# Performance work log

Measured on AMD Instinct MI355X. Metric: run time of the kernel, lower is better.

## Reference

```python
import jax, jax.numpy as jnp
import numpy as np

N_SRC = 100_000
N_DST = 100_000
N_EDGES = 1_600_000
D_IN = 256
N_HEADS = 4
OUT_FEATS = 32
NEG_SLOPE = 0.2


def setup_inputs() -> dict:
    key = jax.random.key(0)
    k1, k2, k3, k4, k5, k6, k7 = jax.random.split(key, 7)
    return {
        "feat_src": jax.random.normal(k1, (N_SRC, D_IN), dtype=jnp.float32),
        "feat_dst": jax.random.normal(k2, (N_DST, D_IN), dtype=jnp.float32),
        "w_src": jax.random.normal(k3, (D_IN, N_HEADS * OUT_FEATS), dtype=jnp.float32) * 0.05,
        "w_dst": jax.random.normal(k4, (D_IN, N_HEADS * OUT_FEATS), dtype=jnp.float32) * 0.05,
        "attn": jax.random.normal(k5, (N_HEADS, 2 * OUT_FEATS), dtype=jnp.float32) * 0.05,
        "src_idx": jax.random.randint(k6, (N_EDGES,), 0, N_SRC, dtype=jnp.int32),
        "dst_idx": jax.random.randint(k7, (N_EDGES,), 0, N_DST, dtype=jnp.int32),
    }


def reference(feat_src, feat_dst, w_src, w_dst, attn, src_idx, dst_idx):
    H, two_d = attn.shape
    D = two_d // 2
    n_dst = feat_dst.shape[0]
    # node transformations (dropout rate = 0.0 -> identity)
    fs = (feat_src @ w_src).reshape(-1, H, D)   # [Ns, H, D]
    fd = (feat_dst @ w_dst).reshape(-1, H, D)   # [Nd, H, D]
    # per-node attention logits: e_dst uses first half, e_src second half
    e_dst = (fd * attn[:, :D]).sum(-1)          # [Nd, H]
    e_src = (fs * attn[:, D:]).sum(-1)          # [Ns, H]
    # u_add_v on edges + leaky relu
    e = e_src[src_idx] + e_dst[dst_idx]         # [E, H]
    e = jnp.where(e > 0, e, NEG_SLOPE * e)
    # edge softmax: segment softmax over incoming edges of each dst node
    m = jax.ops.segment_max(e, dst_idx, num_segments=n_dst)       # [Nd, H]
    m = jnp.where(jnp.isfinite(m), m, 0.0)                        # empty segments
    ex = jnp.exp(e - m[dst_idx])                                  # [E, H]
    denom = jax.ops.segment_sum(ex, dst_idx, num_segments=n_dst)  # [Nd, H]
    a = ex / denom[dst_idx]                                       # [E, H]
    # u_mul_e + sum aggregation
    msg = fs[src_idx] * a[:, :, None]                             # [E, H, D]
    out = jax.ops.segment_sum(msg, dst_idx, num_segments=n_dst)   # [Nd, H, D]
    return jax.nn.relu(out.reshape(n_dst, H * D))
```

## Files before the change

kernel.cpp:

```cpp
#include <hip/hip_runtime.h>

#define N_NODES 100000
#define N_EDGES 1600000
#define D_IN    256
#define HD      128
#define NEG_SLOPE 0.2f

#define BUK_SH    5
#define BUK_NODES 32
#define NBUCKETS ((N_NODES + BUK_NODES - 1) / BUK_NODES)
#define BUK_CAP  1024
#define BUK_CH   8192
#define NB_BUK   ((N_EDGES + BUK_CH - 1) / BUK_CH)
#define NB_PREP 33

#define GEMM_ROWS 128
#define NB_GEMM ((N_NODES + GEMM_ROWS - 1) / GEMM_ROWS)
#define NB_EDST 1024

#define EX_STRIDE 1032

typedef __bf16 bf16x8 __attribute__((ext_vector_type(8)));
typedef float  f32x4  __attribute__((ext_vector_type(4)));

__device__ __forceinline__ float lrelu_exp(float v) {
  v = v > 0.f ? v : NEG_SLOPE * v;
  return __expf(v);
}
__device__ __forceinline__ float bf_lo(unsigned u) { return __uint_as_float(u << 16); }
__device__ __forceinline__ float bf_hi(unsigned u) { return __uint_as_float(u & 0xffff0000u); }

__global__ __launch_bounds__(1024) void prep_bucket_kernel(const float* __restrict__ w_src,
                                                           const float* __restrict__ w_dst,
                                                           const float* __restrict__ attn,
                                                           ushort* __restrict__ wT,
                                                           float* __restrict__ v_dst,
                                                           const int* __restrict__ src,
                                                           const int* __restrict__ dstv,
                                                           int* __restrict__ bcur,
                                                           unsigned* __restrict__ ebuk) {
  const int bid = blockIdx.x;
  const int tid = threadIdx.x;
  if (bid < 32) {
    int idx = bid * 1024 + tid;
    int k = idx >> 7, n = idx & 127;
    __bf16 bv = (__bf16)w_src[idx];
    wT[n * 256 + k] = *(const ushort*)&bv;
  } else if (bid == 32) {
    if (tid < 256) {
      int k = tid;
      for (int h = 0; h < 4; ++h) {
        float s = 0.f;
        for (int d = 0; d < 32; ++d)
          s += w_dst[k * HD + h * 32 + d] * attn[h * 64 + d];
        v_dst[k * 4 + h] = s;
      }
    }
  } else {
    __shared__ int bh[NBUCKETS];
    const int e0 = (bid - NB_PREP) * BUK_CH;
    for (int j = tid; j < NBUCKETS; j += 1024) bh[j] = 0;
    __syncthreads();
    for (int i = tid; i < BUK_CH; i += 1024) {
      int e = e0 + i;
      if (e < N_EDGES) atomicAdd(&bh[dstv[e] >> BUK_SH], 1);
    }
    __syncthreads();
    for (int j = tid; j < NBUCKETS; j += 1024) {
      int c = bh[j];
      bh[j] = (c > 0) ? atomicAdd(&bcur[j], c) : 0;
    }
    __syncthreads();
    for (int i = tid; i < BUK_CH; i += 1024) {
      int e = e0 + i;
      if (e < N_EDGES) {
        int d = dstv[e];
        int b = d >> BUK_SH;
        int p = atomicAdd(&bh[b], 1);
        if (p < BUK_CAP)
          ebuk[(size_t)b * BUK_CAP + p] =
              ((unsigned)src[e] << BUK_SH) | (unsigned)(d & (BUK_NODES - 1));
      }
    }
  }
}

__global__ __launch_bounds__(512, 4) void gemm_kernel(const float* __restrict__ A,
                                                      const ushort* __restrict__ wT16,
                                                      const float* __restrict__ attn,
                                                      unsigned* __restrict__ fs16,
                                                      float* __restrict__ e_src,
                                                      int M) {
  __shared__ ushort Bl[128 * 256];
  const int bid = blockIdx.x;
  const int tid = threadIdx.x;
  const int lane = tid & 63, wid = tid >> 6;
  const int lr = lane & 15, hi = lane >> 4;

  {
    const uint4* wg4 = (const uint4*)wT16;
#pragma unroll
    for (int i = 0; i < 8; ++i) {
      int c = i * 512 + tid;
      int col = c >> 5;
      unsigned byte = ((unsigned)c * 16u) ^ (((unsigned)col & 31u) << 4);
      *(uint4*)((char*)Bl + byte) = wg4[c];
    }
  }

  const int bm = bid * GEMM_ROWS;
  int row0 = bm + wid * 16 + lr;
  int row0c = row0 < M ? row0 : M - 1;
  const float* a0p = A + (size_t)row0c * D_IN;

  float4 u[16];
#pragma unroll
  for (int ks = 0; ks < 8; ++ks) {
    const int ko = ks * 32 + hi * 8;
    u[2 * ks]     = *(const float4*)(a0p + ko);
    u[2 * ks + 1] = *(const float4*)(a0p + ko + 4);
  }

  f32x4 acc[8];
  const f32x4 zf = {0.f, 0.f, 0.f, 0.f};
#pragma unroll
  for (int n = 0; n < 8; ++n) acc[n] = zf;

  __syncthreads();

#pragma unroll
  for (int ks = 0; ks < 8; ++ks) {
    float4 u0 = u[2 * ks], u1 = u[2 * ks + 1];
    bf16x8 af0;
    af0[0] = (__bf16)u0.x; af0[1] = (__bf16)u0.y; af0[2] = (__bf16)u0.z; af0[3] = (__bf16)u0.w;
    af0[4] = (__bf16)u1.x; af0[5] = (__bf16)u1.y; af0[6] = (__bf16)u1.z; af0[7] = (__bf16)u1.w;
    bf16x8 bf[8];
#pragma unroll
    for (int n = 0; n < 8; ++n) {
      unsigned col = (unsigned)(n * 16 + lr);
      unsigned byte = (col * 512u + (unsigned)(ks * 64 + hi * 16)) ^ ((col & 31u) << 4);
      bf[n] = *(const bf16x8*)((const char*)Bl + byte);
    }
#pragma unroll
    for (int n = 0; n < 8; ++n)
      acc[n] = __builtin_amdgcn_mfma_f32_16x16x32_bf16(af0, bf[n], acc[n], 0, 0, 0);
  }

#pragma unroll
  for (int n = 0; n < 8; ++n) {
#pragma unroll
    for (int r4 = 0; r4 < 4; ++r4) {
      float val = acc[n][r4];
      float pv  = __shfl_xor(val, 1, 64);
      int gr = bm + wid * 16 + hi * 4 + r4;
      if (!(lane & 1) && gr < M) {
        __bf16 b0 = (__bf16)val, b1 = (__bf16)pv;
        unsigned pk = ((unsigned)*(const ushort*)&b1 << 16) | *(const ushort*)&b0;
        fs16[(size_t)gr * 64 + n * 8 + (lr >> 1)] = pk;
      }
    }
  }

#pragma unroll
  for (int gh = 0; gh < 4; ++gh) {
    float av0 = attn[gh * 64 + 32 + lr];
    float av1 = attn[gh * 64 + 48 + lr];
#pragma unroll
    for (int r4 = 0; r4 < 4; ++r4) {
      float s = acc[2 * gh][r4] * av0 + acc[2 * gh + 1][r4] * av1;
      s += __shfl_xor(s, 1, 64);
      s += __shfl_xor(s, 2, 64);
      s += __shfl_xor(s, 4, 64);
      s += __shfl_xor(s, 8, 64);
      int gr = bm + wid * 16 + hi * 4 + r4;
      if (lr == 0 && gr < M) e_src[(size_t)gr * 4 + gh] = s;
    }
  }
}

__global__ __launch_bounds__(256) void edst_kernel(const float* __restrict__ feat_dst,
                                                   const float* __restrict__ v_dst,
                                                   float* __restrict__ e_dst) {
  __shared__ float4 vds[256];
  const int tid = threadIdx.x;
  vds[tid] = ((const float4*)v_dst)[tid];
  __syncthreads();
  const int l = tid & 15;
  const int grp = tid >> 4;
  for (int n = blockIdx.x * 16 + grp; n < N_NODES; n += NB_EDST * 16) {
    const float* fp = feat_dst + (size_t)n * D_IN;
    float ax = 0.f, ay = 0.f, az = 0.f, aw = 0.f;
#pragma unroll
    for (int c = 0; c < 4; ++c) {
      const int k0 = c * 64 + l * 4;
      float4 f = *(const float4*)(fp + k0);
      float4 v0 = vds[k0 + 0], v1 = vds[k0 + 1], v2 = vds[k0 + 2], v3 = vds[k0 + 3];
      ax = fmaf(f.x, v0.x, fmaf(f.y, v1.x, fmaf(f.z, v2.x, fmaf(f.w, v3.x, ax))));
      ay = fmaf(f.x, v0.y, fmaf(f.y, v1.y, fmaf(f.z, v2.y, fmaf(f.w, v3.y, ay))));
      az = fmaf(f.x, v0.z, fmaf(f.y, v1.z, fmaf(f.z, v2.z, fmaf(f.w, v3.z, az))));
      aw = fmaf(f.x, v0.w, fmaf(f.y, v1.w, fmaf(f.z, v2.w, fmaf(f.w, v3.w, aw))));
    }
#pragma unroll
    for (int off = 1; off < 16; off <<= 1) {
      ax += __shfl_xor(ax, off, 64);
      ay += __shfl_xor(ay, off, 64);
      az += __shfl_xor(az, off, 64);
      aw += __shfl_xor(aw, off, 64);
    }
    if (l == 0) *(float4*)(e_dst + (size_t)n * 4) = make_float4(ax, ay, az, aw);
  }
}

__global__ __launch_bounds__(256) void agg_kernel(const unsigned* __restrict__ ebuk,
                                                  const int* __restrict__ bcur,
                                                  const float4* __restrict__ e_src,
                                                  const float4* __restrict__ e_dst,
                                                  const unsigned* __restrict__ fs16,
                                                  float* __restrict__ out, int N) {
  __shared__ unsigned sorted_e[BUK_CAP];
  __shared__ float ex_s[4][EX_STRIDE];
  __shared__ int lcnt[BUK_NODES];
  __shared__ int lofs_s[BUK_NODES + 1];
  __shared__ int lcur[BUK_NODES];
  const int tid = threadIdx.x;
  const int wslot = tid >> 6;
  const int lane = tid & 63;
  const int lo = blockIdx.x * BUK_NODES;
  const size_t start = (size_t)blockIdx.x * BUK_CAP;
  const int cnt_e = min(bcur[blockIdx.x], BUK_CAP);

  if (tid < BUK_NODES) lcnt[tid] = 0;
  __syncthreads();
  for (int i = tid; i < cnt_e; i += 256)
    atomicAdd(&lcnt[ebuk[start + i] & (BUK_NODES - 1)], 1);
  __syncthreads();
  if (tid == 0) {
    int run = 0;
    for (int j = 0; j < BUK_NODES; ++j) {
      lofs_s[j] = run; lcur[j] = run; run += lcnt[j];
    }
    lofs_s[BUK_NODES] = run;
  }
  __syncthreads();
  for (int i = tid; i < cnt_e; i += 256) {
    unsigned e = ebuk[start + i];
    int p = atomicAdd(&lcur[e & (BUK_NODES - 1)], 1);
    sorted_e[p] = e;
  }
  __syncthreads();

  for (int i = tid; i < cnt_e; i += 256) {
    unsigned ent = sorted_e[i];
    int s  = (int)(ent >> BUK_SH);
    int dl = (int)(ent & (BUK_NODES - 1));
    float4 a  = e_src[s];
    float4 ed = e_dst[lo + dl];
    ex_s[0][i] = lrelu_exp(a.x + ed.x);
    ex_s[1][i] = lrelu_exp(a.y + ed.y);
    ex_s[2][i] = lrelu_exp(a.z + ed.z);
    ex_s[3][i] = lrelu_exp(a.w + ed.w);
  }
  __syncthreads();

  const int g = lane >> 4;
  const int q = lane & 15;
  const int h = q >> 2;

  for (int nl = wslot * 8; nl < wslot * 8 + 8; ++nl) {
    int node = lo + nl;
    if (node >= N) break;
    const int nb = lofs_s[nl], ne = lofs_s[nl + 1];
    float a0=0.f,a1=0.f,a2=0.f,a3=0.f,a4=0.f,a5=0.f,a6=0.f,a7=0.f,den=0.f;

    for (int cb = nb; cb < ne; cb += 16) {
      int e0 = cb + g, e1 = e0 + 4, e2 = e0 + 8, e3 = e0 + 12;
      bool p0 = e0 < ne, p1 = e1 < ne, p2 = e2 < ne, p3 = e3 < ne;
      int c0 = p0 ? e0 : nb, c1 = p1 ? e1 : nb, c2 = p2 ? e2 : nb, c3 = p3 ? e3 : nb;
      int s0 = (int)(sorted_e[c0] >> BUK_SH);
      int s1 = (int)(sorted_e[c1] >> BUK_SH);
      int s2 = (int)(sorted_e[c2] >> BUK_SH);
      int s3 = (int)(sorted_e[c3] >> BUK_SH);
      uint4 u0 = *(const uint4*)(fs16 + (size_t)s0 * 64 + q * 4);
      uint4 u1 = *(const uint4*)(fs16 + (size_t)s1 * 64 + q * 4);
      uint4 u2 = *(const uint4*)(fs16 + (size_t)s2 * 64 + q * 4);
      uint4 u3 = *(const uint4*)(fs16 + (size_t)s3 * 64 + q * 4);
      float x0 = p0 ? ex_s[h][c0] : 0.f;
      float x1 = p1 ? ex_s[h][c1] : 0.f;
      float x2 = p2 ? ex_s[h][c2] : 0.f;
      float x3 = p3 ? ex_s[h][c3] : 0.f;
      a0 = fmaf(x0, bf_lo(u0.x), a0); a1 = fmaf(x0, bf_hi(u0.x), a1);
      a2 = fmaf(x0, bf_lo(u0.y), a2); a3 = fmaf(x0, bf_hi(u0.y), a3);
      a4 = fmaf(x0, bf_lo(u0.z), a4); a5 = fmaf(x0, bf_hi(u0.z), a5);
      a6 = fmaf(x0, bf_lo(u0.w), a6); a7 = fmaf(x0, bf_hi(u0.w), a7);
      a0 = fmaf(x1, bf_lo(u1.x), a0); a1 = fmaf(x1, bf_hi(u1.x), a1);
      a2 = fmaf(x1, bf_lo(u1.y), a2); a3 = fmaf(x1, bf_hi(u1.y), a3);
      a4 = fmaf(x1, bf_lo(u1.z), a4); a5 = fmaf(x1, bf_hi(u1.z), a5);
      a6 = fmaf(x1, bf_lo(u1.w), a6); a7 = fmaf(x1, bf_hi(u1.w), a7);
      a0 = fmaf(x2, bf_lo(u2.x), a0); a1 = fmaf(x2, bf_hi(u2.x), a1);
      a2 = fmaf(x2, bf_lo(u2.y), a2); a3 = fmaf(x2, bf_hi(u2.y), a3);
      a4 = fmaf(x2, bf_lo(u2.z), a4); a5 = fmaf(x2, bf_hi(u2.z), a5);
      a6 = fmaf(x2, bf_lo(u2.w), a6); a7 = fmaf(x2, bf_hi(u2.w), a7);
      a0 = fmaf(x3, bf_lo(u3.x), a0); a1 = fmaf(x3, bf_hi(u3.x), a1);
      a2 = fmaf(x3, bf_lo(u3.y), a2); a3 = fmaf(x3, bf_hi(u3.y), a3);
      a4 = fmaf(x3, bf_lo(u3.z), a4); a5 = fmaf(x3, bf_hi(u3.z), a5);
      a6 = fmaf(x3, bf_lo(u3.w), a6); a7 = fmaf(x3, bf_hi(u3.w), a7);
      den += x0 + x1 + x2 + x3;
    }

    den += __shfl_xor(den, 16, 64); den += __shfl_xor(den, 32, 64);
    a0 += __shfl_xor(a0, 16, 64); a0 += __shfl_xor(a0, 32, 64);
    a1 += __shfl_xor(a1, 16, 64); a1 += __shfl_xor(a1, 32, 64);
    a2 += __shfl_xor(a2, 16, 64); a2 += __shfl_xor(a2, 32, 64);
    a3 += __shfl_xor(a3, 16, 64); a3 += __shfl_xor(a3, 32, 64);
    a4 += __shfl_xor(a4, 16, 64); a4 += __shfl_xor(a4, 32, 64);
    a5 += __shfl_xor(a5, 16, 64); a5 += __shfl_xor(a5, 32, 64);
    a6 += __shfl_xor(a6, 16, 64); a6 += __shfl_xor(a6, 32, 64);
    a7 += __shfl_xor(a7, 16, 64); a7 += __shfl_xor(a7, 32, 64);
    if (lane < 16) {
      float inv = den > 0.f ? 1.f / den : 0.f;
      float4 o1, o2;
      o1.x = fmaxf(a0 * inv, 0.f); o1.y = fmaxf(a1 * inv, 0.f);
      o1.z = fmaxf(a2 * inv, 0.f); o1.w = fmaxf(a3 * inv, 0.f);
      o2.x = fmaxf(a4 * inv, 0.f); o2.y = fmaxf(a5 * inv, 0.f);
      o2.z = fmaxf(a6 * inv, 0.f); o2.w = fmaxf(a7 * inv, 0.f);
      float* op = out + (size_t)node * HD + q * 8;
      *(float4*)(op)     = o1;
      *(float4*)(op + 4) = o2;
    }
  }
}

extern "C" void kernel_launch(void* const* d_in, const int* in_sizes, int n_in,
                              void* d_out, int out_size, void* d_ws, size_t ws_size,
                              hipStream_t stream) {
  const float* feat_src = (const float*)d_in[0];
  const float* feat_dst = (const float*)d_in[1];
  const float* w_src    = (const float*)d_in[2];
  const float* w_dst    = (const float*)d_in[3];
  const float* attn     = (const float*)d_in[4];
  const int*   src_idx  = (const int*)d_in[5];
  const int*   dst_idx  = (const int*)d_in[6];
  float* out = (float*)d_out;
  char* ws = (char*)d_ws;

  unsigned* fs16  = (unsigned*)(ws);
  float*    e_src = (float*)(ws + 25600000);
  float*    e_dst = (float*)(ws + 27200000);
  unsigned* ebuk  = (unsigned*)(ws + 28800000);
  float*    v_dst = (float*)(ws + 41600000);
  ushort*   wT16  = (ushort*)(ws + 41604096);
  int*      bcur  = (int*)  (ws + 41669632);

  hipMemsetAsync(bcur, 0, NBUCKETS * sizeof(int), stream);

  prep_bucket_kernel<<<NB_PREP + NB_BUK, 1024, 0, stream>>>(
      w_src, w_dst, attn, wT16, v_dst, src_idx, dst_idx, bcur, ebuk);

  gemm_kernel<<<NB_GEMM, 512, 0, stream>>>(feat_src, wT16, attn, fs16, e_src, N_NODES);

  edst_kernel<<<NB_EDST, 256, 0, stream>>>(feat_dst, v_dst, e_dst);

  agg_kernel<<<NBUCKETS, 256, 0, stream>>>(ebuk, bcur,
      (const float4*)e_src, (const float4*)e_dst, fs16, out, N_NODES);
}
```

Measured before the change: 176.5 us.

## Pre-cast feat_src to bf16 MFMA-tiled layout and merge with e_dst kernel

Adds a kernel that converts feat_src to bf16 in an MFMA-fragment-ordered tile layout, staged in the output buffer. The same launch also computes e_dst in separate blocks, replacing the standalone edst kernel. The GEMM then loads bf16 fragments directly with software prefetch, instead of loading fp32 and converting per wave. The cost is an extra full read of feat_src plus a 51 MB write and re-read in exchange for a lighter GEMM and one fewer launch.

```diff
diff --git a/kernel.cpp b/kernel.cpp
--- a/kernel.cpp
+++ b/kernel.cpp
@@ -14,9 +14,11 @@
 #define NB_BUK   ((N_EDGES + BUK_CH - 1) / BUK_CH)
 #define NB_PREP 33
 
+#define NTILES  (N_NODES / 16)
+#define NB_CAST 2048
+#define NB_EDSTB 512
 #define GEMM_ROWS 128
 #define NB_GEMM ((N_NODES + GEMM_ROWS - 1) / GEMM_ROWS)
-#define NB_EDST 1024
 
 #define EX_STRIDE 1032
 
@@ -29,6 +31,10 @@
 }
 __device__ __forceinline__ float bf_lo(unsigned u) { return __uint_as_float(u << 16); }
 __device__ __forceinline__ float bf_hi(unsigned u) { return __uint_as_float(u & 0xffff0000u); }
+__device__ __forceinline__ unsigned pk2(float a, float b) {
+  __bf16 ba = (__bf16)a, bb = (__bf16)b;
+  return ((unsigned)*(const ushort*)&bb << 16) | *(const ushort*)&ba;
+}
 
 __global__ __launch_bounds__(1024) void prep_bucket_kernel(const float* __restrict__ w_src,
                                                            const float* __restrict__ w_dst,
@@ -85,7 +91,59 @@
   }
 }
 
-__global__ __launch_bounds__(512, 4) void gemm_kernel(const float* __restrict__ A,
+__global__ __launch_bounds__(512) void cast_edst_kernel(const float* __restrict__ feat_src,
+                                                        ushort* __restrict__ As,
+                                                        const float* __restrict__ feat_dst,
+                                                        const float* __restrict__ v_dst,
+                                                        float* __restrict__ e_dst) {
+  __shared__ float4 vds[256];
+  const int bid = blockIdx.x;
+  const int tid = threadIdx.x;
+  if (bid < NB_CAST) {
+    const int rl = tid >> 5;
+    const int j  = tid & 31;
+    const int dst_off = (j >> 2) * 64 + (j & 3) * 16 + rl;
+    uint4* Ap = (uint4*)As;
+    for (int t = bid; t < NTILES; t += NB_CAST) {
+      const float* sp = feat_src + ((size_t)t * 16 + rl) * D_IN + j * 8;
+      float4 f0 = *(const float4*)sp;
+      float4 f1 = *(const float4*)(sp + 4);
+      uint4 pk;
+      pk.x = pk2(f0.x, f0.y); pk.y = pk2(f0.z, f0.w);
+      pk.z = pk2(f1.x, f1.y); pk.w = pk2(f1.z, f1.w);
+      Ap[(size_t)t * 512 + dst_off] = pk;
+    }
+  } else {
+    if (tid < 256) vds[tid] = ((const float4*)v_dst)[tid];
+    __syncthreads();
+    const int l = tid & 15;
+    const int grp = tid >> 4;
+    for (int n = (bid - NB_CAST) * 32 + grp; n < N_NODES; n += NB_EDSTB * 32) {
+      const float* fp = feat_dst + (size_t)n * D_IN;
+      float ax = 0.f, ay = 0.f, az = 0.f, aw = 0.f;
+#pragma unroll
+      for (int c = 0; c < 4; ++c) {
+        const int k0 = c * 64 + l * 4;
+        float4 f = *(const float4*)(fp + k0);
+        float4 v0 = vds[k0 + 0], v1 = vds[k0 + 1], v2 = vds[k0 + 2], v3 = vds[k0 + 3];
+        ax = fmaf(f.x, v0.x, fmaf(f.y, v1.x, fmaf(f.z, v2.x, fmaf(f.w, v3.x, ax))));
+        ay = fmaf(f.x, v0.y, fmaf(f.y, v1.y, fmaf(f.z, v2.y, fmaf(f.w, v3.y, ay))));
+        az = fmaf(f.x, v0.z, fmaf(f.y, v1.z, fmaf(f.z, v2.z, fmaf(f.w, v3.z, az))));
+        aw = fmaf(f.x, v0.w, fmaf(f.y, v1.w, fmaf(f.z, v2.w, fmaf(f.w, v3.w, aw))));
+      }
+#pragma unroll
+      for (int off = 1; off < 16; off <<= 1) {
+        ax += __shfl_xor(ax, off, 64);
+        ay += __shfl_xor(ay, off, 64);
+        az += __shfl_xor(az, off, 64);
+        aw += __shfl_xor(aw, off, 64);
+      }
+      if (l == 0) *(float4*)(e_dst + (size_t)n * 4) = make_float4(ax, ay, az, aw);
+    }
+  }
+}
+
+__global__ __launch_bounds__(512, 4) void gemm_kernel(const ushort* __restrict__ As,
                                                       const ushort* __restrict__ wT16,
                                                       const float* __restrict__ attn,
                                                       unsigned* __restrict__ fs16,
@@ -108,18 +166,11 @@
     }
   }
 
-  const int bm = bid * GEMM_ROWS;
-  int row0 = bm + wid * 16 + lr;
-  int row0c = row0 < M ? row0 : M - 1;
-  const float* a0p = A + (size_t)row0c * D_IN;
-
-  float4 u[16];
-#pragma unroll
-  for (int ks = 0; ks < 8; ++ks) {
-    const int ko = ks * 32 + hi * 8;
-    u[2 * ks]     = *(const float4*)(a0p + ko);
-    u[2 * ks + 1] = *(const float4*)(a0p + ko + 4);
-  }
+  int tile = bid * 8 + wid;
+  if (tile >= NTILES) tile = NTILES - 1;
+  const bf16x8* ap = (const bf16x8*)As + (size_t)tile * 512 + lane;
+
+  bf16x8 afc = ap[0];
 
   f32x4 acc[8];
   const f32x4 zf = {0.f, 0.f, 0.f, 0.f};
@@ -130,10 +181,8 @@
 
 #pragma unroll
   for (int ks = 0; ks < 8; ++ks) {
-    float4 u0 = u[2 * ks], u1 = u[2 * ks + 1];
-    bf16x8 af0;
-    af0[0] = (__bf16)u0.x; af0[1] = (__bf16)u0.y; af0[2] = (__bf16)u0.z; af0[3] = (__bf16)u0.w;
-    af0[4] = (__bf16)u1.x; af0[5] = (__bf16)u1.y; af0[6] = (__bf16)u1.z; af0[7] = (__bf16)u1.w;
+    bf16x8 afn = afc;
+    if (ks < 7) afn = ap[(ks + 1) * 64];
     bf16x8 bf[8];
 #pragma unroll
     for (int n = 0; n < 8; ++n) {
@@ -143,8 +192,11 @@
     }
 #pragma unroll
     for (int n = 0; n < 8; ++n)
-      acc[n] = __builtin_amdgcn_mfma_f32_16x16x32_bf16(af0, bf[n], acc[n], 0, 0, 0);
-  }
+      acc[n] = __builtin_amdgcn_mfma_f32_16x16x32_bf16(afc, bf[n], acc[n], 0, 0, 0);
+    afc = afn;
+  }
+
+  const int bm = bid * GEMM_ROWS;
 
 #pragma unroll
   for (int n = 0; n < 8; ++n) {
@@ -175,39 +227,6 @@
       int gr = bm + wid * 16 + hi * 4 + r4;
       if (lr == 0 && gr < M) e_src[(size_t)gr * 4 + gh] = s;
     }
-  }
-}
-
-__global__ __launch_bounds__(256) void edst_kernel(const float* __restrict__ feat_dst,
-                                                   const float* __restrict__ v_dst,
-                                                   float* __restrict__ e_dst) {
-  __shared__ float4 vds[256];
-  const int tid = threadIdx.x;
-  vds[tid] = ((const float4*)v_dst)[tid];
-  __syncthreads();
-  const int l = tid & 15;
-  const int grp = tid >> 4;
-  for (int n = blockIdx.x * 16 + grp; n < N_NODES; n += NB_EDST * 16) {
-    const float* fp = feat_dst + (size_t)n * D_IN;
-    float ax = 0.f, ay = 0.f, az = 0.f, aw = 0.f;
-#pragma unroll
-    for (int c = 0; c < 4; ++c) {
-      const int k0 = c * 64 + l * 4;
-      float4 f = *(const float4*)(fp + k0);
-      float4 v0 = vds[k0 + 0], v1 = vds[k0 + 1], v2 = vds[k0 + 2], v3 = vds[k0 + 3];
-      ax = fmaf(f.x, v0.x, fmaf(f.y, v1.x, fmaf(f.z, v2.x, fmaf(f.w, v3.x, ax))));
-      ay = fmaf(f.x, v0.y, fmaf(f.y, v1.y, fmaf(f.z, v2.y, fmaf(f.w, v3.y, ay))));
-      az = fmaf(f.x, v0.z, fmaf(f.y, v1.z, fmaf(f.z, v2.z, fmaf(f.w, v3.z, az))));
-      aw = fmaf(f.x, v0.w, fmaf(f.y, v1.w, fmaf(f.z, v2.w, fmaf(f.w, v3.w, aw))));
-    }
-#pragma unroll
-    for (int off = 1; off < 16; off <<= 1) {
-      ax += __shfl_xor(ax, off, 64);
-      ay += __shfl_xor(ay, off, 64);
-      az += __shfl_xor(az, off, 64);
-      aw += __shfl_xor(aw, off, 64);
-    }
-    if (l == 0) *(float4*)(e_dst + (size_t)n * 4) = make_float4(ax, ay, az, aw);
   }
 }
 
@@ -351,14 +370,17 @@
   ushort*   wT16  = (ushort*)(ws + 41604096);
   int*      bcur  = (int*)  (ws + 41669632);
 
+  ushort* As = (ushort*)d_out;
+
   hipMemsetAsync(bcur, 0, NBUCKETS * sizeof(int), stream);
 
   prep_bucket_kernel<<<NB_PREP + NB_BUK, 1024, 0, stream>>>(
       w_src, w_dst, attn, wT16, v_dst, src_idx, dst_idx, bcur, ebuk);
 
-  gemm_kernel<<<NB_GEMM, 512, 0, stream>>>(feat_src, wT16, attn, fs16, e_src, N_NODES);
-
-  edst_kernel<<<NB_EDST, 256, 0, stream>>>(feat_dst, v_dst, e_dst);
+  cast_edst_kernel<<<NB_CAST + NB_EDSTB, 512, 0, stream>>>(
+      feat_src, As, feat_dst, v_dst, e_dst);
+
+  gemm_kernel<<<NB_GEMM, 512, 0, stream>>>(As, wT16, attn, fs16, e_src, N_NODES);
 
   agg_kernel<<<NBUCKETS, 256, 0, stream>>>(ebuk, bcur,
       (const float4*)e_src, (const float4*)e_dst, fs16, out, N_NODES);
```

After: 194.2 us. +10.0%, slower.
